# Performance work log

Hardware: AMD Instinct MI355X
Metric: run time of the kernel (lower is better)

## Reference

```python
import jax, jax.numpy as jnp
import numpy as np

EMBED_SIZE = 1024

def setup_inputs() -> dict:
    key = jax.random.key(0)
    k1, k2, k3, k4 = jax.random.split(key, 4)
    B, T, C, H = 8, 2048, 1024, 128
    embeddings = jax.random.normal(k1, (B, T, C), dtype=jnp.float32)
    # nn.Linear(embed, head, bias=False) weight applied as x @ W^T; store as [C, H] for x @ W
    scale = 1.0 / np.sqrt(C)
    Wq = jax.random.normal(k2, (C, H), dtype=jnp.float32) * scale
    Wk = jax.random.normal(k3, (C, H), dtype=jnp.float32) * scale
    Wv = jax.random.normal(k4, (C, H), dtype=jnp.float32) * scale
    return {"embeddings": embeddings, "Wq": Wq, "Wk": Wk, "Wv": Wv}

def reference(embeddings, Wq, Wk, Wv):
    B, T, C = embeddings.shape
    q = jnp.einsum('btc,ch->bth', embeddings, Wq)
    k = jnp.einsum('btc,ch->bth', embeddings, Wk)
    v = jnp.einsum('btc,ch->bth', embeddings, Wv)
    # NOTE: source scales by embed_size**-0.5 (not head_size**-0.5)
    wei = jnp.einsum('bqh,bkh->bqk', q, k) * (C ** -0.5)
    causal = jnp.tril(jnp.ones((T, T), dtype=bool))  # tril buffer
    wei = jnp.where(causal, wei, -jnp.inf)
    wei = jax.nn.softmax(wei, axis=-1)
    return jnp.einsum('bqk,bkh->bqh', wei, v)
```

## Files before the change

### kernel.cpp

```cpp
#include <hip/hip_runtime.h>
#include <hip/hip_bf16.h>

typedef __bf16 bf16x8 __attribute__((ext_vector_type(8)));
typedef float f32x4 __attribute__((ext_vector_type(4)));
typedef ushort us8 __attribute__((ext_vector_type(8)));

#define MFMA(a, b, c) __builtin_amdgcn_mfma_f32_16x16x32_bf16((a), (b), (c), 0, 0, 0)

static constexpr int T_LEN = 2048;
static constexpr int C_DIM = 1024;
static constexpr int H_DIM = 128;
static constexpr int M_ROWS = 8 * 2048;
static constexpr int N_COLS = 384;
static constexpr int SLOTS_PER_B = 528;
static constexpr int PSTR = 72;
static constexpr int KSTR = 136;
static constexpr int VSTR = 72;

__device__ __forceinline__ ushort f2bf(float f) {
  union { float f; unsigned u; } v; v.f = f;
  unsigned u = v.u;
  u += 0x7fffu + ((u >> 16) & 1u);
  return (ushort)(u >> 16);
}
__device__ __forceinline__ float bf2f(ushort u) {
  union { unsigned u; float f; } v; v.u = (unsigned)u << 16;
  return v.f;
}

__device__ __forceinline__ void waitbar() {
  asm volatile("s_waitcnt lgkmcnt(0)" ::: "memory");
  __builtin_amdgcn_s_barrier();
  __builtin_amdgcn_sched_barrier(0);
}

__device__ __forceinline__ int sw128(int row, int slot) {
  return row * 128 + ((slot * 16) ^ ((row & 7) << 4));
}

__global__ void wt_convert(const float* __restrict__ Wq,
                           const float* __restrict__ Wk,
                           const float* __restrict__ Wv,
                           ushort* __restrict__ wt) {
  int o = blockIdx.x * 256 + threadIdx.x;
  int kt = o / 24576;
  int rem = o - kt * 24576;
  int gc = rem >> 6;
  int kk = rem & 63;
  int c  = kt * 64 + kk;
  int mat = gc >> 7;
  int h   = gc & 127;
  const float* W = (mat == 0) ? Wq : ((mat == 1) ? Wk : Wv);
  wt[o] = f2bf(W[c * H_DIM + h]);
}

__global__ __launch_bounds__(256, 2) void qkv_gemm(const float* __restrict__ X,
                                                   const ushort* __restrict__ wt,
                                                   ushort* __restrict__ qws,
                                                   ushort* __restrict__ kws,
                                                   ushort* __restrict__ vtws) {
  __shared__ ushort As[2][64 * 64];
  __shared__ ushort Bs[2][192 * 64];
  const int tid = threadIdx.x;
  const int wid = tid >> 6, lane = tid & 63;
  const int lg = lane >> 4, lr = lane & 15;
  const int m0 = (blockIdx.x >> 1) * 64;
  const int n0 = (blockIdx.x & 1) * 192;
  const float QSCL = 0.03125f * 1.44269504f;

  const int arow = tid >> 3, aslot = tid & 7;
  const float* gA0 = &X[(size_t)(m0 + arow) * C_DIM + aslot * 8];
  const float* gA1 = gA0 + (size_t)32 * C_DIM;
  const int awb0 = sw128(arow, aslot);
  const ushort* gBt = wt + (size_t)n0 * 64 + (size_t)tid * 8;
  const int bwb0 = sw128(tid >> 3, tid & 7);

  const int afb0 = sw128(lr, lg), afb1 = sw128(lr, 4 + lg);
  const int bfb0 = sw128(wid * 48 + lr, lg), bfb1 = sw128(wid * 48 + lr, 4 + lg);

  f32x4 acc[4][3];
#pragma unroll
  for (int r = 0; r < 4; ++r)
#pragma unroll
    for (int c = 0; c < 3; ++c)
      acc[r][c] = f32x4{0.f, 0.f, 0.f, 0.f};

  float4 aE[4], aO[4];
  us8 bE[6], bO[6];

#define LOAD_SET(aS, bS, kt_)                                              \
  {                                                                        \
    aS[0] = *(const float4*)(gA0 + (kt_) * 64);                            \
    aS[1] = *(const float4*)(gA0 + (kt_) * 64 + 4);                        \
    aS[2] = *(const float4*)(gA1 + (kt_) * 64);                            \
    aS[3] = *(const float4*)(gA1 + (kt_) * 64 + 4);                        \
    const ushort* gB_ = gBt + (size_t)(kt_) * 24576;                       \
    bS[0] = *(const us8*)(gB_);                                            \
    bS[1] = *(const us8*)(gB_ + 2048);                                     \
    bS[2] = *(const us8*)(gB_ + 4096);                                     \
    bS[3] = *(const us8*)(gB_ + 6144);                                     \
    bS[4] = *(const us8*)(gB_ + 8192);                                     \
    bS[5] = *(const us8*)(gB_ + 10240);                                    \
  }

#define WRITE_SET(aS, bS, buf)                                             \
  {                                                                        \
    us8 av0, av1;                                                          \
    av0[0] = f2bf(aS[0].x); av0[1] = f2bf(aS[0].y);                        \
    av0[2] = f2bf(aS[0].z); av0[3] = f2bf(aS[0].w);                        \
    av0[4] = f2bf(aS[1].x); av0[5] = f2bf(aS[1].y);                        \
    av0[6] = f2bf(aS[1].z); av0[7] = f2bf(aS[1].w);                        \
    av1[0] = f2bf(aS[2].x); av1[1] = f2bf(aS[2].y);                        \
    av1[2] = f2bf(aS[2].z); av1[3] = f2bf(aS[2].w);                        \
    av1[4] = f2bf(aS[3].x); av1[5] = f2bf(aS[3].y);                        \
    av1[6] = f2bf(aS[3].z); av1[7] = f2bf(aS[3].w);                        \
    *(us8*)((char*)&As[buf][0] + awb0) = av0;                              \
    *(us8*)((char*)&As[buf][0] + awb0 + 4096) = av1;                       \
    _Pragma("unroll")                                                      \
    for (int i = 0; i < 6; ++i)                                            \
      *(us8*)((char*)&Bs[buf][0] + bwb0 + i * 4096) = bS[i];               \
  }

#define COMPUTE(buf)                                                       \
  {                                                                        \
    _Pragma("unroll")                                                      \
    for (int kk = 0; kk < 2; ++kk) {                                       \
      const int afb = kk ? afb1 : afb0;                                    \
      const int bfb = kk ? bfb1 : bfb0;                                    \
      bf16x8 a0 = *(const bf16x8*)((const char*)&As[buf][0] + afb);        \
      bf16x8 a1 = *(const bf16x8*)((const char*)&As[buf][0] + afb + 2048); \
      bf16x8 a2 = *(const bf16x8*)((const char*)&As[buf][0] + afb + 4096); \
      bf16x8 a3 = *(const bf16x8*)((const char*)&As[buf][0] + afb + 6144); \
      _Pragma("unroll")                                                    \
      for (int c = 0; c < 3; ++c) {                                        \
        bf16x8 bf = *(const bf16x8*)((const char*)&Bs[buf][0] + bfb + c * 2048); \
        acc[0][c] = MFMA(a0, bf, acc[0][c]);                               \
        acc[1][c] = MFMA(a1, bf, acc[1][c]);                               \
        acc[2][c] = MFMA(a2, bf, acc[2][c]);                               \
        acc[3][c] = MFMA(a3, bf, acc[3][c]);                               \
      }                                                                    \
    }                                                                      \
  }

  {
    float4 aT[4];
    us8 bT[6];
    LOAD_SET(aT, bT, 0);
    WRITE_SET(aT, bT, 0);
  }
  LOAD_SET(aE, bE, 1);
  LOAD_SET(aO, bO, 2);
  waitbar();

  for (int k2 = 0; k2 < 16; k2 += 2) {
    WRITE_SET(aE, bE, 1);
    if (k2 + 3 < 16) LOAD_SET(aE, bE, k2 + 3);
    COMPUTE(0);
    waitbar();

    if (k2 + 2 < 16) WRITE_SET(aO, bO, 0);
    if (k2 + 4 < 16) LOAD_SET(aO, bO, k2 + 4);
    COMPUTE(1);
    waitbar();
  }
#undef LOAD_SET
#undef WRITE_SET
#undef COMPUTE

#pragma unroll
  for (int c = 0; c < 3; ++c) {
    int gc = n0 + wid * 48 + c * 16 + lr;
    int mat = gc >> 7, h = gc & 127;
#pragma unroll
    for (int r = 0; r < 4; ++r) {
#pragma unroll
      for (int j = 0; j < 4; ++j) {
        int gr = m0 + r * 16 + lg * 4 + j;
        float val = acc[r][c][j];
        ushort ov = f2bf(mat == 0 ? val * QSCL : val);
        if (mat == 0) {
          qws[(size_t)gr * H_DIM + h] = ov;
        } else if (mat == 1) {
          kws[(size_t)gr * H_DIM + h] = ov;
        } else {
          int b = gr >> 11, t = gr & 2047;
          vtws[((size_t)b * H_DIM + h) * T_LEN + t] = ov;
        }
      }
    }
  }
}

__global__ __launch_bounds__(256, 3) void attn_part(const ushort* __restrict__ qws,
                                                    const ushort* __restrict__ kws,
                                                    const ushort* __restrict__ vtws,
                                                    float* __restrict__ pml,
                                                    ushort* __restrict__ pacc,
                                                    float* __restrict__ out) {
  __shared__ ushort Klds[64 * KSTR];
  __shared__ ushort Vlds[128 * VSTR];
  __shared__ ushort Pw[4][16 * PSTR];

  const int tid = threadIdx.x;
  const int wid = tid >> 6, lane = tid & 63;
  const int lg = lane >> 4, lr = lane & 15;
  const int bid = blockIdx.x;
  const int b = bid & 7;
  const int item = bid >> 3;

  int qb, ck;
  bool direct;
  if (item < 8) {
    qb = item; ck = 0; direct = true;
  } else {
    const int p = item - 8;
    direct = false;
    if (p < 12)      { int q = p / 3;        qb = 8 + q;  ck = p - q * 3; }
    else if (p < 28) { int q = (p - 12) >> 2; qb = 12 + q; ck = (p - 12) & 3; }
    else if (p < 48) { int q = (p - 28) / 5; qb = 16 + q; ck = (p - 28) - q * 5; }
    else if (p < 72) { int q = (p - 48) / 6; qb = 20 + q; ck = (p - 48) - q * 6; }
    else if (p < 100){ int q = (p - 72) / 7; qb = 24 + q; ck = (p - 72) - q * 7; }
    else             { int q = (p - 100) >> 3; qb = 28 + q; ck = (p - 100) & 7; }
  }
  const int qi = qb * 4 + wid;
  const int q0 = qi * 16;
  const int nt = qb + 1;
  const int kvt_lo = direct ? 0 : ck * 4;
  const int kvt_hi = direct ? nt : min(ck * 4 + 4, nt);
  const size_t tokbase = (size_t)b * T_LEN;
  const ushort* vb = vtws + (size_t)b * H_DIM * T_LEN;

  const int kr = tid >> 2, kseg = tid & 3;
  const int vr = tid >> 1, vseg = tid & 1;
  const ushort* gK = &kws[(tokbase + kr) * H_DIM + kseg * 32];
  const ushort* gV = &vb[(size_t)vr * T_LEN + vseg * 32];

  bf16x8 qf[4];
#pragma unroll
  for (int hk = 0; hk < 4; ++hk)
    qf[hk] = *(const bf16x8*)&qws[(tokbase + q0 + lr) * H_DIM + hk * 32 + lg * 8];

  f32x4 acc[8];
#pragma unroll
  for (int hf = 0; hf < 8; ++hf) acc[hf] = f32x4{0.f, 0.f, 0.f, 0.f};
  float mrun = -INFINITY, lrun = 0.f;

  ushort* Pme = &Pw[wid][0];

  us8 kreg[4], vreg[4];
#pragma unroll
  for (int i = 0; i < 4; ++i) {
    kreg[i] = *(const us8*)(gK + (size_t)kvt_lo * 64 * H_DIM + i * 8);
    vreg[i] = *(const us8*)(gV + kvt_lo * 64 + i * 8);
  }

  for (int kvt = kvt_lo; kvt < kvt_hi; ++kvt) {
    const int kv0 = kvt * 64;

    __syncthreads();
#pragma unroll
    for (int i = 0; i < 4; ++i) {
      *(us8*)&Klds[kr * KSTR + kseg * 32 + i * 8] = kreg[i];
      *(us8*)&Vlds[vr * VSTR + vseg * 32 + i * 8] = vreg[i];
    }
    if (kvt + 1 < kvt_hi) {
#pragma unroll
      for (int i = 0; i < 4; ++i) {
        kreg[i] = *(const us8*)(gK + (size_t)(kv0 + 64) * H_DIM + i * 8);
        vreg[i] = *(const us8*)(gV + kv0 + 64 + i * 8);
      }
    }
    __syncthreads();

    f32x4 s[4];
#pragma unroll
    for (int c = 0; c < 4; ++c) {
      f32x4 sc = f32x4{0.f, 0.f, 0.f, 0.f};
#pragma unroll
      for (int hk = 0; hk < 4; ++hk) {
        bf16x8 kf = *(const bf16x8*)&Klds[(c * 16 + lr) * KSTR + hk * 32 + lg * 8];
        sc = MFMA(kf, qf[hk], sc);
      }
      s[c] = sc;
    }

    if (kvt == nt - 1) {
#pragma unroll
      for (int c = 0; c < 4; ++c)
#pragma unroll
        for (int j = 0; j < 4; ++j) {
          int kv = kv0 + c * 16 + lg * 4 + j;
          if (kv > q0 + lr) s[c][j] = -INFINITY;
        }
    }

    float mx = s[0][0];
#pragma unroll
    for (int c = 0; c < 4; ++c)
#pragma unroll
      for (int j = 0; j < 4; ++j) mx = fmaxf(mx, s[c][j]);
    mx = fmaxf(mx, __shfl_xor(mx, 16));
    mx = fmaxf(mx, __shfl_xor(mx, 32));

    float mnew = fmaxf(mrun, mx);
    float scold = exp2f(mrun - mnew);

    float rsum = 0.f;
#pragma unroll
    for (int c = 0; c < 4; ++c)
#pragma unroll
      for (int j = 0; j < 4; ++j) {
        float p = exp2f(s[c][j] - mnew);
        s[c][j] = p;
        rsum += p;
      }

#pragma unroll
    for (int c = 0; c < 4; ++c) {
      ushort4 u;
      u.x = f2bf(s[c][0]); u.y = f2bf(s[c][1]);
      u.z = f2bf(s[c][2]); u.w = f2bf(s[c][3]);
      *(ushort4*)&Pme[lr * PSTR + c * 16 + lg * 4] = u;
    }

    bf16x8 v0[8];
#pragma unroll
    for (int hf = 0; hf < 8; ++hf)
      v0[hf] = *(const bf16x8*)&Vlds[(hf * 16 + lr) * VSTR + lg * 8];

    rsum += __shfl_xor(rsum, 16);
    rsum += __shfl_xor(rsum, 32);

    lrun = lrun * scold + rsum;
    mrun = mnew;
#pragma unroll
    for (int hf = 0; hf < 8; ++hf)
#pragma unroll
      for (int j = 0; j < 4; ++j) acc[hf][j] *= scold;

    bf16x8 pa0 = *(const bf16x8*)&Pme[lr * PSTR + lg * 8];
    bf16x8 pa1 = *(const bf16x8*)&Pme[lr * PSTR + 32 + lg * 8];

#pragma unroll
    for (int hf = 0; hf < 8; ++hf)
      acc[hf] = MFMA(v0[hf], pa0, acc[hf]);
#pragma unroll
    for (int hf = 0; hf < 8; ++hf) {
      bf16x8 v1 = *(const bf16x8*)&Vlds[(hf * 16 + lr) * VSTR + 32 + lg * 8];
      acc[hf] = MFMA(v1, pa1, acc[hf]);
    }
  }

  if (direct) {
    float inv = 1.0f / lrun;
    float* op = &out[(tokbase + q0 + lr) * H_DIM + lg * 4];
#pragma unroll
    for (int hf = 0; hf < 8; ++hf) {
      float4 r0 = make_float4(acc[hf][0] * inv, acc[hf][1] * inv,
                              acc[hf][2] * inv, acc[hf][3] * inv);
      *(float4*)(op + hf * 16) = r0;
    }
  } else {
    int base;
    if (qi < 48)       base = (qi - 32) * 3;
    else if (qi < 64)  base = 48 + (qi - 48) * 4;
    else if (qi < 80)  base = 112 + (qi - 64) * 5;
    else if (qi < 96)  base = 192 + (qi - 80) * 6;
    else if (qi < 112) base = 288 + (qi - 96) * 7;
    else               base = 400 + (qi - 112) * 8;
    const size_t slot = (size_t)b * SLOTS_PER_B + base + ck;
    if (lg == 0) {
      pml[slot * 32 + lr] = mrun;
      pml[slot * 32 + 16 + lr] = lrun;
    }
    ushort* ap = &pacc[slot * 2048 + (size_t)lr * 128 + lg * 4];
#pragma unroll
    for (int hf = 0; hf < 8; ++hf) {
      ushort4 u;
      u.x = f2bf(acc[hf][0]); u.y = f2bf(acc[hf][1]);
      u.z = f2bf(acc[hf][2]); u.w = f2bf(acc[hf][3]);
      *(ushort4*)(ap + hf * 16) = u;
    }
  }
}

__global__ __launch_bounds__(256) void attn_merge(const float* __restrict__ pml,
                                                  const ushort* __restrict__ pacc,
                                                  float* __restrict__ out) {
  const int bid = blockIdx.x;
  const int b = bid & 7, qi = (bid >> 3) + 32;
  int base, nch;
  if (qi < 48)       { base = (qi - 32) * 3;        nch = 3; }
  else if (qi < 64)  { base = 48 + (qi - 48) * 4;   nch = 4; }
  else if (qi < 80)  { base = 112 + (qi - 64) * 5;  nch = 5; }
  else if (qi < 96)  { base = 192 + (qi - 80) * 6;  nch = 6; }
  else if (qi < 112) { base = 288 + (qi - 96) * 7;  nch = 7; }
  else               { base = 400 + (qi - 112) * 8; nch = 8; }
  const size_t slot0 = (size_t)b * SLOTS_PER_B + base;
  const int tid = threadIdx.x;
  const int r = tid >> 4, c0 = (tid & 15) * 8;

  float mrun = -INFINITY, L = 0.f;
  float o[8];
#pragma unroll
  for (int i = 0; i < 8; ++i) o[i] = 0.f;

  for (int ck = 0; ck < nch; ++ck) {
    const size_t s = slot0 + ck;
    float m = pml[s * 32 + r];
    float l = pml[s * 32 + 16 + r];
    float mn = fmaxf(mrun, m);
    float sc = exp2f(mrun - mn);
    float w  = exp2f(m - mn);
    L = L * sc + w * l;
    const ushort* ap = &pacc[s * 2048 + (size_t)r * 128 + c0];
    ushort4 u0 = *(const ushort4*)ap;
    ushort4 u1 = *(const ushort4*)(ap + 4);
    o[0] = o[0] * sc + w * bf2f(u0.x); o[1] = o[1] * sc + w * bf2f(u0.y);
    o[2] = o[2] * sc + w * bf2f(u0.z); o[3] = o[3] * sc + w * bf2f(u0.w);
    o[4] = o[4] * sc + w * bf2f(u1.x); o[5] = o[5] * sc + w * bf2f(u1.y);
    o[6] = o[6] * sc + w * bf2f(u1.z); o[7] = o[7] * sc + w * bf2f(u1.w);
    mrun = mn;
  }
  float invL = 1.0f / L;
  float4 r0 = make_float4(o[0] * invL, o[1] * invL, o[2] * invL, o[3] * invL);
  float4 r1 = make_float4(o[4] * invL, o[5] * invL, o[6] * invL, o[7] * invL);
  float* op = &out[((size_t)b * T_LEN + qi * 16 + r) * H_DIM + c0];
  *(float4*)op = r0;
  *(float4*)(op + 4) = r1;
}

extern "C" void kernel_launch(void* const* d_in, const int* in_sizes, int n_in,
                              void* d_out, int out_size, void* d_ws, size_t ws_size,
                              hipStream_t stream) {
  const float* emb = (const float*)d_in[0];
  const float* Wq  = (const float*)d_in[1];
  const float* Wk  = (const float*)d_in[2];
  const float* Wv  = (const float*)d_in[3];
  float* out = (float*)d_out;

  ushort* wt   = (ushort*)d_ws;
  ushort* qws  = wt  + (size_t)N_COLS * C_DIM;
  ushort* kws  = qws + (size_t)M_ROWS * H_DIM;
  ushort* vtws = kws + (size_t)M_ROWS * H_DIM;
  ushort* pacc = vtws + (size_t)8 * H_DIM * T_LEN;
  float*  pml  = (float*)d_ws;

  wt_convert<<<(N_COLS * C_DIM) / 256, 256, 0, stream>>>(Wq, Wk, Wv, wt);
  qkv_gemm<<<(M_ROWS / 64) * 2, 256, 0, stream>>>(emb, wt, qws, kws, vtws);
  attn_part<<<8 * 140, 256, 0, stream>>>(qws, kws, vtws, pml, pacc, out);
  attn_merge<<<8 * 96, 256, 0, stream>>>(pml, pacc, out);
}
```

Measured before the change: 79.47 us.

## Stage QKV weight tiles directly into LDS via global_load_lds with fragment-ordered layout

Reorders the pre-converted bf16 weight buffer so each 512-element chunk matches one MFMA B-fragment lane layout, then loads B tiles straight from global memory into LDS with global_load_lds instead of through registers. Synchronization switches to explicit vmcnt waits, and the k-loop is restructured into a single-step loop with a peeled tail. This cuts VGPR pressure and register-to-LDS store instructions in the QKV GEMM, at the cost of a more delicate vmcnt accounting that must match the in-flight load count.

```diff
diff --git a/kernel.cpp b/kernel.cpp
--- a/kernel.cpp
+++ b/kernel.cpp
@@ -28,28 +28,37 @@
   return v.f;
 }
 
-__device__ __forceinline__ void waitbar() {
-  asm volatile("s_waitcnt lgkmcnt(0)" ::: "memory");
-  __builtin_amdgcn_s_barrier();
-  __builtin_amdgcn_sched_barrier(0);
+__device__ __forceinline__ void gl2lds16(const ushort* g, ushort* l) {
+  __builtin_amdgcn_global_load_lds(
+      (const __attribute__((address_space(1))) unsigned int*)(const void*)g,
+      (__attribute__((address_space(3))) unsigned int*)(void*)l, 16, 0, 0);
 }
 
 __device__ __forceinline__ int sw128(int row, int slot) {
   return row * 128 + ((slot * 16) ^ ((row & 7) << 4));
 }
+
+#define SYNCV(VMC)                                                   \
+  asm volatile("s_waitcnt vmcnt(" #VMC ")" ::: "memory");            \
+  asm volatile("s_waitcnt lgkmcnt(0)" ::: "memory");                 \
+  __builtin_amdgcn_s_barrier();                                      \
+  __builtin_amdgcn_sched_barrier(0);
 
 __global__ void wt_convert(const float* __restrict__ Wq,
                            const float* __restrict__ Wk,
                            const float* __restrict__ Wv,
                            ushort* __restrict__ wt) {
   int o = blockIdx.x * 256 + threadIdx.x;
-  int kt = o / 24576;
-  int rem = o - kt * 24576;
-  int gc = rem >> 6;
-  int kk = rem & 63;
-  int c  = kt * 64 + kk;
-  int mat = gc >> 7;
-  int h   = gc & 127;
+  int kthalf = o / 12288;
+  int rem = o - kthalf * 12288;
+  int fs = rem >> 9;
+  int li = rem & 511;
+  int lane = li >> 3, j = li & 7;
+  int kt = kthalf >> 1, half = kthalf & 1;
+  int kk = fs / 12, cg = fs - kk * 12;
+  int gc = half * 192 + cg * 16 + (lane & 15);
+  int c  = kt * 64 + kk * 32 + (lane >> 4) * 8 + j;
+  int mat = gc >> 7, h = gc & 127;
   const float* W = (mat == 0) ? Wq : ((mat == 1) ? Wk : Wv);
   wt[o] = f2bf(W[c * H_DIM + h]);
 }
@@ -60,23 +69,21 @@
                                                    ushort* __restrict__ kws,
                                                    ushort* __restrict__ vtws) {
   __shared__ ushort As[2][64 * 64];
-  __shared__ ushort Bs[2][192 * 64];
+  __shared__ ushort Bs[2][24 * 512];
   const int tid = threadIdx.x;
   const int wid = tid >> 6, lane = tid & 63;
   const int lg = lane >> 4, lr = lane & 15;
   const int m0 = (blockIdx.x >> 1) * 64;
-  const int n0 = (blockIdx.x & 1) * 192;
+  const int n0h = blockIdx.x & 1;
+  const int n0 = n0h * 192;
   const float QSCL = 0.03125f * 1.44269504f;
 
   const int arow = tid >> 3, aslot = tid & 7;
   const float* gA0 = &X[(size_t)(m0 + arow) * C_DIM + aslot * 8];
   const float* gA1 = gA0 + (size_t)32 * C_DIM;
   const int awb0 = sw128(arow, aslot);
-  const ushort* gBt = wt + (size_t)n0 * 64 + (size_t)tid * 8;
-  const int bwb0 = sw128(tid >> 3, tid & 7);
 
   const int afb0 = sw128(lr, lg), afb1 = sw128(lr, 4 + lg);
-  const int bfb0 = sw128(wid * 48 + lr, lg), bfb1 = sw128(wid * 48 + lr, 4 + lg);
 
   f32x4 acc[4][3];
 #pragma unroll
@@ -86,24 +93,15 @@
       acc[r][c] = f32x4{0.f, 0.f, 0.f, 0.f};
 
   float4 aE[4], aO[4];
-  us8 bE[6], bO[6];
-
-#define LOAD_SET(aS, bS, kt_)                                              \
+
+#define LOAD_A(aS, kt_)                                                    \
   {                                                                        \
     aS[0] = *(const float4*)(gA0 + (kt_) * 64);                            \
     aS[1] = *(const float4*)(gA0 + (kt_) * 64 + 4);                        \
     aS[2] = *(const float4*)(gA1 + (kt_) * 64);                            \
     aS[3] = *(const float4*)(gA1 + (kt_) * 64 + 4);                        \
-    const ushort* gB_ = gBt + (size_t)(kt_) * 24576;                       \
-    bS[0] = *(const us8*)(gB_);                                            \
-    bS[1] = *(const us8*)(gB_ + 2048);                                     \
-    bS[2] = *(const us8*)(gB_ + 4096);                                     \
-    bS[3] = *(const us8*)(gB_ + 6144);                                     \
-    bS[4] = *(const us8*)(gB_ + 8192);                                     \
-    bS[5] = *(const us8*)(gB_ + 10240);                                    \
-  }
-
-#define WRITE_SET(aS, bS, buf)                                             \
+  }
+#define WRITE_A(aS, buf)                                                   \
   {                                                                        \
     us8 av0, av1;                                                          \
     av0[0] = f2bf(aS[0].x); av0[1] = f2bf(aS[0].y);                        \
@@ -116,24 +114,29 @@
     av1[6] = f2bf(aS[3].z); av1[7] = f2bf(aS[3].w);                        \
     *(us8*)((char*)&As[buf][0] + awb0) = av0;                              \
     *(us8*)((char*)&As[buf][0] + awb0 + 4096) = av1;                       \
+  }
+#define STAGE_B(kt_, buf_)                                                 \
+  {                                                                        \
+    const ushort* gB_ = wt + (size_t)(((kt_) * 2 + n0h) * 24) * 512        \
+                          + (size_t)lane * 8;                              \
     _Pragma("unroll")                                                      \
-    for (int i = 0; i < 6; ++i)                                            \
-      *(us8*)((char*)&Bs[buf][0] + bwb0 + i * 4096) = bS[i];               \
-  }
-
+    for (int jj = 0; jj < 6; ++jj)                                         \
+      gl2lds16(gB_ + (size_t)(wid + 4 * jj) * 512,                         \
+               &Bs[buf_][(wid + 4 * jj) * 512]);                           \
+  }
 #define COMPUTE(buf)                                                       \
   {                                                                        \
     _Pragma("unroll")                                                      \
     for (int kk = 0; kk < 2; ++kk) {                                       \
       const int afb = kk ? afb1 : afb0;                                    \
-      const int bfb = kk ? bfb1 : bfb0;                                    \
       bf16x8 a0 = *(const bf16x8*)((const char*)&As[buf][0] + afb);        \
       bf16x8 a1 = *(const bf16x8*)((const char*)&As[buf][0] + afb + 2048); \
       bf16x8 a2 = *(const bf16x8*)((const char*)&As[buf][0] + afb + 4096); \
       bf16x8 a3 = *(const bf16x8*)((const char*)&As[buf][0] + afb + 6144); \
       _Pragma("unroll")                                                    \
       for (int c = 0; c < 3; ++c) {                                        \
-        bf16x8 bf = *(const bf16x8*)((const char*)&Bs[buf][0] + bfb + c * 2048); \
+        bf16x8 bf = *(const bf16x8*)&Bs[buf][(kk * 12 + wid * 3 + c) * 512 \
+                                            + lane * 8];                   \
         acc[0][c] = MFMA(a0, bf, acc[0][c]);                               \
         acc[1][c] = MFMA(a1, bf, acc[1][c]);                               \
         acc[2][c] = MFMA(a2, bf, acc[2][c]);                               \
@@ -142,29 +145,38 @@
     }                                                                      \
   }
 
+  STAGE_B(0, 0);
   {
     float4 aT[4];
-    us8 bT[6];
-    LOAD_SET(aT, bT, 0);
-    WRITE_SET(aT, bT, 0);
-  }
-  LOAD_SET(aE, bE, 1);
-  LOAD_SET(aO, bO, 2);
-  waitbar();
-
-  for (int k2 = 0; k2 < 16; k2 += 2) {
-    WRITE_SET(aE, bE, 1);
-    if (k2 + 3 < 16) LOAD_SET(aE, bE, k2 + 3);
-    COMPUTE(0);
-    waitbar();
-
-    if (k2 + 2 < 16) WRITE_SET(aO, bO, 0);
-    if (k2 + 4 < 16) LOAD_SET(aO, bO, k2 + 4);
-    COMPUTE(1);
-    waitbar();
-  }
-#undef LOAD_SET
-#undef WRITE_SET
+    LOAD_A(aT, 0);
+    WRITE_A(aT, 0);
+  }
+  LOAD_A(aE, 1);
+  LOAD_A(aO, 2);
+  SYNCV(8);
+
+  for (int kt = 0; kt < 13; ++kt) {
+    const int cur = kt & 1;
+    STAGE_B(kt + 1, cur ^ 1);
+    if (kt & 1) { WRITE_A(aO, cur ^ 1); LOAD_A(aO, kt + 3); }
+    else        { WRITE_A(aE, cur ^ 1); LOAD_A(aE, kt + 3); }
+    COMPUTE(cur);
+    SYNCV(4);
+  }
+
+  STAGE_B(14, 0);
+  WRITE_A(aO, 0);
+  COMPUTE(1);
+  SYNCV(0);
+  STAGE_B(15, 1);
+  WRITE_A(aE, 1);
+  COMPUTE(0);
+  SYNCV(0);
+  COMPUTE(1);
+
+#undef LOAD_A
+#undef WRITE_A
+#undef STAGE_B
 #undef COMPUTE
 
 #pragma unroll
```

Measured after the change: 77.94 us. No clear change (-1.9%).
